# Kernel tuning notes

Measured on AMD Instinct MI355X. Metric: run time of the kernel, lower is better.

Reference implementation:

```python
import jax, jax.numpy as jnp
import numpy as np

NEG = -1e9  # effectively -inf for masked logits, grad-safe

def apply_rope(t, cos, sin):
    # t: [b, H, S, D]; cos/sin: [S, D] -> rotate-half RoPE
    d = t.shape[-1]
    t1, t2 = t[..., : d // 2], t[..., d // 2 :]
    rot = jnp.concatenate([-t2, t1], axis=-1)
    return t * cos[None, None] + rot * sin[None, None]


def setup_inputs() -> dict:
    key = jax.random.key(0)
    ks = jax.random.split(key, 8)
    b, S, d_in = 1, 4096, 2048
    H, G, D = 16, 4, 128
    d_out = H * D
    sc = 1.0 / np.sqrt(d_in)
    x = jax.random.normal(ks[0], (b, S, d_in), dtype=jnp.float32)
    # causal mask: True = masked (future positions)
    mask = jnp.triu(jnp.ones((S, S), dtype=bool), k=1)
    inv = 1.0 / (10000.0 ** (jnp.arange(0, D, 2, dtype=jnp.float32) / D))
    ang = jnp.arange(S, dtype=jnp.float32)[:, None] * inv[None, :]  # [S, D/2]
    ang = jnp.concatenate([ang, ang], axis=-1)                      # [S, D]
    cos, sin = jnp.cos(ang), jnp.sin(ang)
    Wq = jax.random.normal(ks[1], (d_out, d_in), dtype=jnp.float32) * sc
    Wk = jax.random.normal(ks[2], (G * D, d_in), dtype=jnp.float32) * sc
    Wv = jax.random.normal(ks[3], (G * D, d_in), dtype=jnp.float32) * sc
    Wo = jax.random.normal(ks[4], (d_in, d_out), dtype=jnp.float32) * sc
    return {"x": x, "mask": mask, "cos": cos, "sin": sin,
            "Wq": Wq, "Wk": Wk, "Wv": Wv, "Wo": Wo}


def reference(x, mask, cos, sin, Wq, Wk, Wv, Wo):
    b, S, d_in = x.shape
    G = Wk.shape[0] // cos.shape[-1]          # num_kv_groups
    D = cos.shape[-1]                          # head_dim
    H = Wq.shape[0] // D                       # num_heads
    n = H // G                                 # group_size
    q = (x @ Wq.T).reshape(b, S, H, D).transpose(0, 2, 1, 3)   # [b,H,S,D]
    k = (x @ Wk.T).reshape(b, S, G, D).transpose(0, 2, 1, 3)   # [b,G,S,D]
    v = (x @ Wv.T).reshape(b, S, G, D).transpose(0, 2, 1, 3)
    q = apply_rope(q, cos, sin)
    k = apply_rope(k, cos, sin)
    # GQA: group heads instead of repeat_interleave (head h -> group h // n)
    qg = q.reshape(b, G, n, S, D)
    scores = jnp.einsum('bgnqd,bgkd->bgnqk', qg, k)            # [b,G,n,S,S]
    scores = jnp.where(mask[None, None, None], NEG, scores)
    w = jax.nn.softmax(scores / np.sqrt(D), axis=-1)
    ctx = jnp.einsum('bgnqk,bgkd->bgnqd', w, v)                # [b,G,n,S,D]
    ctx = ctx.reshape(b, H, S, D).transpose(0, 2, 1, 3).reshape(b, S, H * D)
    return ctx @ Wo.T
```

## Files before the change

kernel.cpp:

```cpp
#include <hip/hip_runtime.h>

typedef __attribute__((ext_vector_type(8))) short bf16x8;
typedef __attribute__((ext_vector_type(4))) short bf16x4;
typedef __attribute__((ext_vector_type(8))) unsigned short u16x8;
typedef __attribute__((ext_vector_type(4))) float f32x4;

__device__ __forceinline__ unsigned short f2b(float f) {
  unsigned int u = __builtin_bit_cast(unsigned int, f);
  u += 0x7FFFu + ((u >> 16) & 1u);
  return (unsigned short)(u >> 16);
}
__device__ __forceinline__ float b2f(unsigned short h) {
  return __builtin_bit_cast(float, ((unsigned int)h) << 16);
}

__device__ __forceinline__ f32x4 mfma16x16x16(bf16x4 a, bf16x4 b, f32x4 c) {
#if __has_builtin(__builtin_amdgcn_mfma_f32_16x16x16bf16_1k)
  return __builtin_amdgcn_mfma_f32_16x16x16bf16_1k(a, b, c, 0, 0, 0);
#else
  asm volatile("v_mfma_f32_16x16x16_bf16 %0, %1, %2, %0" : "+v"(c) : "v"(a), "v"(b));
  return c;
#endif
}

#define AS1(p) (const __attribute__((address_space(1))) void*)(p)
#define AS3(p) (__attribute__((address_space(3))) void*)(p)

__device__ __forceinline__ void cvt8(const float* __restrict__ in,
                                     unsigned short* __restrict__ out,
                                     int i, float scale) {
  const float4* p = (const float4*)in + (size_t)i * 2;
  float4 a = p[0], b = p[1];
  u16x8 r;
  r[0] = f2b(a.x * scale); r[1] = f2b(a.y * scale);
  r[2] = f2b(a.z * scale); r[3] = f2b(a.w * scale);
  r[4] = f2b(b.x * scale); r[5] = f2b(b.y * scale);
  r[6] = f2b(b.z * scale); r[7] = f2b(b.w * scale);
  *((u16x8*)out + i) = r;
}

__global__ __launch_bounds__(256) void k_cvt_all(
    const float* __restrict__ x,  const float* __restrict__ Wq,
    const float* __restrict__ Wk, const float* __restrict__ Wv,
    const float* __restrict__ Wo, unsigned short* __restrict__ xb,
    unsigned short* __restrict__ wqkv, unsigned short* __restrict__ Wob,
    float sc) {
  int bid = blockIdx.x;
  int tid = threadIdx.x;
  if (bid < 4096)      cvt8(x,  xb,             (bid        ) * 256 + tid, 1.f);
  else if (bid < 6144) cvt8(Wq, wqkv,           (bid - 4096) * 256 + tid, sc);
  else if (bid < 6656) cvt8(Wk, wqkv + 4194304, (bid - 6144) * 256 + tid, 1.f);
  else if (bid < 7168) cvt8(Wv, wqkv + 5242880, (bid - 6656) * 256 + tid, 1.f);
  else                 cvt8(Wo, Wob,            (bid - 7168) * 256 + tid, 1.f);
}

__global__ __launch_bounds__(256) void k_post(unsigned short* __restrict__ qkv,
                                              const float* __restrict__ cosb,
                                              const float* __restrict__ sinb,
                                              unsigned short* __restrict__ vT) {
  __shared__ unsigned short tile[64][72];
  const int bid = blockIdx.x, t = threadIdx.x;
  if (bid < 2560) {
    int tid = bid * 256 + t;
    int oct = tid & 7;
    int hd  = (tid >> 3) % 20;
    int s   = (tid >> 3) / 20;
    unsigned short* p1 = qkv + (size_t)s * 3072 + hd * 128 + oct * 8;
    unsigned short* p2 = p1 + 64;
    u16x8 a = *(const u16x8*)p1;
    u16x8 b = *(const u16x8*)p2;
    const float4* cp = (const float4*)(cosb + (size_t)s * 128 + oct * 8);
    const float4* sp = (const float4*)(sinb + (size_t)s * 128 + oct * 8);
    float4 c0 = cp[0], c1 = cp[1], s0 = sp[0], s1 = sp[1];
    float cs[8] = {c0.x,c0.y,c0.z,c0.w,c1.x,c1.y,c1.z,c1.w};
    float sn[8] = {s0.x,s0.y,s0.z,s0.w,s1.x,s1.y,s1.z,s1.w};
    u16x8 ra, rb;
#pragma unroll
    for (int j = 0; j < 8; ++j) {
      float av = b2f(a[j]), bv = b2f(b[j]);
      ra[j] = f2b(av * cs[j] - bv * sn[j]);
      rb[j] = f2b(bv * cs[j] + av * sn[j]);
    }
    *(u16x8*)p1 = ra;
    *(u16x8*)p2 = rb;
  } else {
    int idx = bid - 2560;
    int bs = idx >> 3, bc = idx & 7;
#pragma unroll
    for (int i = 0; i < 2; ++i) {
      int c8 = t + 256 * i;
      int row = c8 >> 3, cb = c8 & 7;
      u16x8 v = *(const u16x8*)(qkv + (size_t)(bs * 64 + row) * 3072 + 2560 + bc * 64 + cb * 8);
#pragma unroll
      for (int j = 0; j < 8; ++j) tile[row][cb * 8 + j] = v[j];
    }
    __syncthreads();
#pragma unroll
    for (int i = 0; i < 2; ++i) {
      int c8 = t + 256 * i;
      int crow = c8 >> 3, sb = c8 & 7;
      u16x8 v;
#pragma unroll
      for (int j = 0; j < 8; ++j) v[j] = tile[sb * 8 + j][crow];
      *(u16x8*)(vT + (size_t)(bc * 64 + crow) * 4096 + bs * 64 + sb * 8) = v;
    }
  }
}

template <int OUTF32>
__global__ __launch_bounds__(256) void k_gemm_bt(
    const unsigned short* __restrict__ A, const unsigned short* __restrict__ B,
    void* __restrict__ C, int K, int lda, int ldb, int ldc) {
  __shared__ unsigned short As[128 * 64];
  __shared__ unsigned short Bs[128 * 64];
  const int t = threadIdx.x;
  const int lane = t & 63, w = t >> 6;
  const int wm = w >> 1, wn = w & 1;
  const int bn = blockIdx.x, bm = blockIdx.y;
  const unsigned short* Arow = A + (size_t)(bm * 128) * lda;
  const unsigned short* Brow = B + (size_t)(bn * 128) * ldb;

  f32x4 acc[4][4] = {};
  for (int kt = 0; kt < K; kt += 64) {
#pragma unroll
    for (int i = 0; i < 4; ++i) {
      int idx = i * 256 + t;
      int r = idx >> 3, blk = idx & 7;
      int sb = blk ^ (r & 7);
      __builtin_amdgcn_global_load_lds(AS1(Arow + (size_t)r * lda + kt + sb * 8),
                                       AS3(As + (i * 256 + w * 64) * 8), 16, 0, 0);
    }
#pragma unroll
    for (int i = 0; i < 4; ++i) {
      int idx = i * 256 + t;
      int r = idx >> 3, blk = idx & 7;
      int sb = blk ^ (r & 7);
      __builtin_amdgcn_global_load_lds(AS1(Brow + (size_t)r * ldb + kt + sb * 8),
                                       AS3(Bs + (i * 256 + w * 64) * 8), 16, 0, 0);
    }
    __syncthreads();
#pragma unroll
    for (int kk = 0; kk < 2; ++kk) {
      bf16x8 av[4], bv[4];
#pragma unroll
      for (int i = 0; i < 4; ++i) {
        int r = wm * 64 + i * 16 + (lane & 15);
        int off = (r * 128 + (kk * 32 + (lane >> 4) * 8) * 2) ^ ((r & 7) << 4);
        av[i] = *(const bf16x8*)((const char*)As + off);
      }
#pragma unroll
      for (int j = 0; j < 4; ++j) {
        int r = wn * 64 + j * 16 + (lane & 15);
        int off = (r * 128 + (kk * 32 + (lane >> 4) * 8) * 2) ^ ((r & 7) << 4);
        bv[j] = *(const bf16x8*)((const char*)Bs + off);
      }
#pragma unroll
      for (int i = 0; i < 4; ++i)
#pragma unroll
        for (int j = 0; j < 4; ++j)
          acc[i][j] = __builtin_amdgcn_mfma_f32_16x16x32_bf16(av[i], bv[j], acc[i][j], 0, 0, 0);
    }
    __syncthreads();
  }
#pragma unroll
  for (int i = 0; i < 4; ++i)
#pragma unroll
    for (int j = 0; j < 4; ++j)
#pragma unroll
      for (int r = 0; r < 4; ++r) {
        int m = bm * 128 + wm * 64 + i * 16 + (lane >> 4) * 4 + r;
        int n = bn * 128 + wn * 64 + j * 16 + (lane & 15);
        float v = acc[i][j][r];
        if (OUTF32) ((float*)C)[(size_t)m * ldc + n] = v;
        else        ((unsigned short*)C)[(size_t)m * ldc + n] = f2b(v);
      }
}

__device__ __forceinline__ void stage_k(const unsigned short* __restrict__ qk,
                                        unsigned short* __restrict__ dst,
                                        int kt, int g, int t, int w) {
#pragma unroll
  for (int i = 0; i < 4; ++i) {
    int idx = i * 256 + t;
    int r = idx >> 4, blk = idx & 15;
    int sb = (blk & 8) | ((blk ^ r) & 7);
    __builtin_amdgcn_global_load_lds(
        AS1(qk + (size_t)(kt * 64 + r) * 3072 + 2048 + g * 128 + sb * 8),
        AS3(dst + (i * 256 + w * 64) * 8), 16, 0, 0);
  }
}
__device__ __forceinline__ void stage_v(const unsigned short* __restrict__ vT,
                                        unsigned short* __restrict__ dst,
                                        int kt, int g, int t, int w) {
#pragma unroll
  for (int i = 0; i < 4; ++i) {
    int idx = i * 256 + t;
    int r = idx >> 3, blk = idx & 7;
    int sb = blk ^ (r & 7);
    __builtin_amdgcn_global_load_lds(
        AS1(vT + (size_t)(g * 128 + r) * 4096 + kt * 64 + sb * 8),
        AS3(dst + (i * 256 + w * 64) * 8), 16, 0, 0);
  }
}

__global__ __launch_bounds__(256, 1) void k_attn(const unsigned short* __restrict__ qk,
                                                 const unsigned short* __restrict__ vT,
                                                 unsigned short* __restrict__ ctx) {
  __shared__ unsigned short Ks[2][64 * 128];
  __shared__ unsigned short Vs[2][64 * 128];
  const int b = blockIdx.x;
  const int hp = blockIdx.y;
  const int h0 = hp * 2, g = hp >> 1;
  const int t = threadIdx.x, lane = t & 63, w = t >> 6;
  const int l15 = lane & 15, lq = lane >> 4;

  for (int ph = 0; ph < 2; ++ph) {
    const int qt = ph ? 63 - b : b;
    const int qg = qt * 64 + w * 16 + l15;

    bf16x8 aq0[4], aq1[4];
    {
      const unsigned short* qb =
          qk + (size_t)(qt * 64 + w * 16 + l15) * 3072 + h0 * 128 + lq * 8;
#pragma unroll
      for (int sl = 0; sl < 4; ++sl) {
        aq0[sl] = *(const bf16x8*)(qb + sl * 32);
        aq1[sl] = *(const bf16x8*)(qb + 128 + sl * 32);
      }
    }
    f32x4 o0[8] = {}, o1[8] = {};
    float lsum0 = 0.f, lsum1 = 0.f;

    stage_k(qk, Ks[0], 0, g, t, w);
    stage_v(vT, Vs[0], 0, g, t, w);
    asm volatile("s_waitcnt vmcnt(0)" ::: "memory");
    __builtin_amdgcn_s_barrier();

    auto tile = [&](const unsigned short* Kb, const unsigned short* Vb,
                    int kt, bool maskT) {
      f32x4 st0[4] = {}, st1[4] = {};
      __builtin_amdgcn_s_setprio(1);
#pragma unroll
      for (int sl = 0; sl < 4; ++sl)
#pragma unroll
        for (int nt = 0; nt < 4; ++nt) {
          int key = nt * 16 + l15;
          int off = (key * 256 + sl * 64 + lq * 16) ^ ((key & 7) << 4);
          bf16x8 bk = *(const bf16x8*)((const char*)Kb + off);
          st0[nt] = __builtin_amdgcn_mfma_f32_16x16x32_bf16(bk, aq0[sl], st0[nt], 0, 0, 0);
          st1[nt] = __builtin_amdgcn_mfma_f32_16x16x32_bf16(bk, aq1[sl], st1[nt], 0, 0, 0);
        }
      __builtin_amdgcn_s_setprio(0);

      bf16x4 pa0[4], pa1[4];
#pragma unroll
      for (int nt = 0; nt < 4; ++nt)
#pragma unroll
        for (int r = 0; r < 4; ++r) {
          float p0 = __builtin_amdgcn_exp2f(st0[nt][r]);
          float p1 = __builtin_amdgcn_exp2f(st1[nt][r]);
          if (maskT) {
            int key = kt * 64 + nt * 16 + lq * 4 + r;
            if (key > qg) { p0 = 0.f; p1 = 0.f; }
          }
          lsum0 += p0; lsum1 += p1;
          unsigned int u0 = __builtin_bit_cast(unsigned int, p0) + 0x8000u;
          unsigned int u1 = __builtin_bit_cast(unsigned int, p1) + 0x8000u;
          pa0[nt][r] = (short)(u0 >> 16);
          pa1[nt][r] = (short)(u1 >> 16);
        }

      __builtin_amdgcn_s_setprio(1);
#pragma unroll
      for (int nt = 0; nt < 4; ++nt)
#pragma unroll
        for (int dt = 0; dt < 8; ++dt) {
          int d = dt * 16 + l15;
          int off = (d * 128 + nt * 32 + lq * 8) ^ ((d & 7) << 4);
          bf16x4 vv = *(const bf16x4*)((const char*)Vb + off);
          o0[dt] = mfma16x16x16(pa0[nt], vv, o0[dt]);
          o1[dt] = mfma16x16x16(pa1[nt], vv, o1[dt]);
        }
      __builtin_amdgcn_s_setprio(0);
    };

    for (int kt = 0; kt < qt; ++kt) {
      const int cur = kt & 1;
      stage_k(qk, Ks[cur ^ 1], kt + 1, g, t, w);
      stage_v(vT, Vs[cur ^ 1], kt + 1, g, t, w);
      tile(Ks[cur], Vs[cur], kt, false);
      asm volatile("s_waitcnt vmcnt(0)" ::: "memory");
      __builtin_amdgcn_s_barrier();
    }
    {
      tile(Ks[qt & 1], Vs[qt & 1], qt, true);
      __builtin_amdgcn_s_barrier();
    }

    float f0 = lsum0, f1 = lsum1;
    f0 += __shfl_xor(f0, 16); f0 += __shfl_xor(f0, 32);
    f1 += __shfl_xor(f1, 16); f1 += __shfl_xor(f1, 32);
    float iq0[4], iq1[4];
#pragma unroll
    for (int r = 0; r < 4; ++r) {
      iq0[r] = 1.f / __shfl(f0, lq * 4 + r);
      iq1[r] = 1.f / __shfl(f1, lq * 4 + r);
    }
#pragma unroll
    for (int dt = 0; dt < 8; ++dt)
#pragma unroll
      for (int r = 0; r < 4; ++r) {
        int q = qt * 64 + w * 16 + lq * 4 + r;
        int c = h0 * 128 + dt * 16 + l15;
        ctx[(size_t)q * 2048 + c]       = f2b(o0[dt][r] * iq0[r]);
        ctx[(size_t)q * 2048 + c + 128] = f2b(o1[dt][r] * iq1[r]);
      }
  }
}

extern "C" void kernel_launch(void* const* d_in, const int* in_sizes, int n_in,
                              void* d_out, int out_size, void* d_ws, size_t ws_size,
                              hipStream_t stream) {
  const float* x    = (const float*)d_in[0];
  const float* cosb = (const float*)d_in[2];
  const float* sinb = (const float*)d_in[3];
  const float* Wq   = (const float*)d_in[4];
  const float* Wk   = (const float*)d_in[5];
  const float* Wv   = (const float*)d_in[6];
  const float* Wo   = (const float*)d_in[7];

  char* p = (char*)d_ws;
  unsigned short* xb   = (unsigned short*)p; p += (size_t)8388608 * 2;
  unsigned short* wqkv = (unsigned short*)p; p += (size_t)6291456 * 2;
  unsigned short* Wob  = (unsigned short*)p; p += (size_t)4194304 * 2;
  unsigned short* qkvb = (unsigned short*)p; p += (size_t)4096 * 3072 * 2;
  unsigned short* vTb  = (unsigned short*)p; p += (size_t)512 * 4096 * 2;
  unsigned short* ctx  = (unsigned short*)p; p += (size_t)4096 * 2048 * 2;
  if (ws_size < (size_t)(p - (char*)d_ws)) return;

  const float SC = 0.12751741f;

  k_cvt_all<<<9216, 256, 0, stream>>>(x, Wq, Wk, Wv, Wo, xb, wqkv, Wob, SC);

  k_gemm_bt<0><<<dim3(24, 32), 256, 0, stream>>>(xb, wqkv, qkvb, 2048, 2048, 2048, 3072);

  k_post<<<3072, 256, 0, stream>>>(qkvb, cosb, sinb, vTb);

  k_attn<<<dim3(32, 8), 256, 0, stream>>>(qkvb, vTb, ctx);

  k_gemm_bt<1><<<dim3(16, 32), 256, 0, stream>>>(ctx, Wob, d_out, 2048, 2048, 2048, 2048);
}
```

Measured before the change: 263.6 us.

## Process both paired causal query tiles concurrently with 512-thread attention blocks

The attention kernel now launches 512 threads per block, with waves 0-3 handling query tile b and waves 4-7 handling the paired tile 63-b at the same time, instead of processing the two tiles one after another. The K/V tiles staged into shared memory are loaded once and shared by both query tiles, which halves K/V global traffic for the short tile and doubles the waves available to hide latency. In exchange, the waves on the short tile sit idle at barriers once they pass their diagonal. Register pressure per wave is unchanged, but launch_bounds(512,1) may constrain the compiler's register allocation.

```diff
diff --git a/kernel.cpp b/kernel.cpp
--- a/kernel.cpp
+++ b/kernel.cpp
@@ -176,34 +176,34 @@
       }
 }
 
-__device__ __forceinline__ void stage_k(const unsigned short* __restrict__ qk,
-                                        unsigned short* __restrict__ dst,
-                                        int kt, int g, int t, int w) {
-#pragma unroll
-  for (int i = 0; i < 4; ++i) {
-    int idx = i * 256 + t;
+__device__ __forceinline__ void stage_k8(const unsigned short* __restrict__ qk,
+                                         unsigned short* __restrict__ dst,
+                                         int kt, int g, int t, int w) {
+#pragma unroll
+  for (int i = 0; i < 2; ++i) {
+    int idx = i * 512 + t;
     int r = idx >> 4, blk = idx & 15;
     int sb = (blk & 8) | ((blk ^ r) & 7);
     __builtin_amdgcn_global_load_lds(
         AS1(qk + (size_t)(kt * 64 + r) * 3072 + 2048 + g * 128 + sb * 8),
-        AS3(dst + (i * 256 + w * 64) * 8), 16, 0, 0);
-  }
-}
-__device__ __forceinline__ void stage_v(const unsigned short* __restrict__ vT,
-                                        unsigned short* __restrict__ dst,
-                                        int kt, int g, int t, int w) {
-#pragma unroll
-  for (int i = 0; i < 4; ++i) {
-    int idx = i * 256 + t;
+        AS3(dst + (i * 512 + w * 64) * 8), 16, 0, 0);
+  }
+}
+__device__ __forceinline__ void stage_v8(const unsigned short* __restrict__ vT,
+                                         unsigned short* __restrict__ dst,
+                                         int kt, int g, int t, int w) {
+#pragma unroll
+  for (int i = 0; i < 2; ++i) {
+    int idx = i * 512 + t;
     int r = idx >> 3, blk = idx & 7;
     int sb = blk ^ (r & 7);
     __builtin_amdgcn_global_load_lds(
         AS1(vT + (size_t)(g * 128 + r) * 4096 + kt * 64 + sb * 8),
-        AS3(dst + (i * 256 + w * 64) * 8), 16, 0, 0);
-  }
-}
-
-__global__ __launch_bounds__(256, 1) void k_attn(const unsigned short* __restrict__ qk,
+        AS3(dst + (i * 512 + w * 64) * 8), 16, 0, 0);
+  }
+}
+
+__global__ __launch_bounds__(512, 1) void k_attn(const unsigned short* __restrict__ qk,
                                                  const unsigned short* __restrict__ vT,
                                                  unsigned short* __restrict__ ctx) {
   __shared__ unsigned short Ks[2][64 * 128];
@@ -212,110 +212,108 @@
   const int hp = blockIdx.y;
   const int h0 = hp * 2, g = hp >> 1;
   const int t = threadIdx.x, lane = t & 63, w = t >> 6;
+  const int wq = w & 3;
+  const int myqt = (w < 4) ? b : 63 - b;
+  const int kmax = 63 - b;
   const int l15 = lane & 15, lq = lane >> 4;
-
-  for (int ph = 0; ph < 2; ++ph) {
-    const int qt = ph ? 63 - b : b;
-    const int qg = qt * 64 + w * 16 + l15;
-
-    bf16x8 aq0[4], aq1[4];
-    {
-      const unsigned short* qb =
-          qk + (size_t)(qt * 64 + w * 16 + l15) * 3072 + h0 * 128 + lq * 8;
-#pragma unroll
-      for (int sl = 0; sl < 4; ++sl) {
-        aq0[sl] = *(const bf16x8*)(qb + sl * 32);
-        aq1[sl] = *(const bf16x8*)(qb + 128 + sl * 32);
-      }
-    }
-    f32x4 o0[8] = {}, o1[8] = {};
-    float lsum0 = 0.f, lsum1 = 0.f;
-
-    stage_k(qk, Ks[0], 0, g, t, w);
-    stage_v(vT, Vs[0], 0, g, t, w);
+  const int qg = myqt * 64 + wq * 16 + l15;
+
+  bf16x8 aq0[4], aq1[4];
+  {
+    const unsigned short* qb =
+        qk + (size_t)(myqt * 64 + wq * 16 + l15) * 3072 + h0 * 128 + lq * 8;
+#pragma unroll
+    for (int sl = 0; sl < 4; ++sl) {
+      aq0[sl] = *(const bf16x8*)(qb + sl * 32);
+      aq1[sl] = *(const bf16x8*)(qb + 128 + sl * 32);
+    }
+  }
+  f32x4 o0[8] = {}, o1[8] = {};
+  float lsum0 = 0.f, lsum1 = 0.f;
+
+  stage_k8(qk, Ks[0], 0, g, t, w);
+  stage_v8(vT, Vs[0], 0, g, t, w);
+  asm volatile("s_waitcnt vmcnt(0)" ::: "memory");
+  __builtin_amdgcn_s_barrier();
+
+  auto tile = [&](const unsigned short* Kb, const unsigned short* Vb,
+                  int kt, bool maskT) {
+    f32x4 st0[4] = {}, st1[4] = {};
+    __builtin_amdgcn_s_setprio(1);
+#pragma unroll
+    for (int sl = 0; sl < 4; ++sl)
+#pragma unroll
+      for (int nt = 0; nt < 4; ++nt) {
+        int key = nt * 16 + l15;
+        int off = (key * 256 + sl * 64 + lq * 16) ^ ((key & 7) << 4);
+        bf16x8 bk = *(const bf16x8*)((const char*)Kb + off);
+        st0[nt] = __builtin_amdgcn_mfma_f32_16x16x32_bf16(bk, aq0[sl], st0[nt], 0, 0, 0);
+        st1[nt] = __builtin_amdgcn_mfma_f32_16x16x32_bf16(bk, aq1[sl], st1[nt], 0, 0, 0);
+      }
+    __builtin_amdgcn_s_setprio(0);
+
+    bf16x4 pa0[4], pa1[4];
+#pragma unroll
+    for (int nt = 0; nt < 4; ++nt)
+#pragma unroll
+      for (int r = 0; r < 4; ++r) {
+        float p0 = __builtin_amdgcn_exp2f(st0[nt][r]);
+        float p1 = __builtin_amdgcn_exp2f(st1[nt][r]);
+        if (maskT) {
+          int key = kt * 64 + nt * 16 + lq * 4 + r;
+          if (key > qg) { p0 = 0.f; p1 = 0.f; }
+        }
+        lsum0 += p0; lsum1 += p1;
+        unsigned int u0 = __builtin_bit_cast(unsigned int, p0) + 0x8000u;
+        unsigned int u1 = __builtin_bit_cast(unsigned int, p1) + 0x8000u;
+        pa0[nt][r] = (short)(u0 >> 16);
+        pa1[nt][r] = (short)(u1 >> 16);
+      }
+
+    __builtin_amdgcn_s_setprio(1);
+#pragma unroll
+    for (int nt = 0; nt < 4; ++nt)
+#pragma unroll
+      for (int dt = 0; dt < 8; ++dt) {
+        int d = dt * 16 + l15;
+        int off = (d * 128 + nt * 32 + lq * 8) ^ ((d & 7) << 4);
+        bf16x4 vv = *(const bf16x4*)((const char*)Vb + off);
+        o0[dt] = mfma16x16x16(pa0[nt], vv, o0[dt]);
+        o1[dt] = mfma16x16x16(pa1[nt], vv, o1[dt]);
+      }
+    __builtin_amdgcn_s_setprio(0);
+  };
+
+  for (int kt = 0; kt <= kmax; ++kt) {
+    const int cur = kt & 1;
+    if (kt < kmax) {
+      stage_k8(qk, Ks[cur ^ 1], kt + 1, g, t, w);
+      stage_v8(vT, Vs[cur ^ 1], kt + 1, g, t, w);
+    }
+    if (kt <= myqt)
+      tile(Ks[cur], Vs[cur], kt, kt == myqt);
     asm volatile("s_waitcnt vmcnt(0)" ::: "memory");
     __builtin_amdgcn_s_barrier();
-
-    auto tile = [&](const unsigned short* Kb, const unsigned short* Vb,
-                    int kt, bool maskT) {
-      f32x4 st0[4] = {}, st1[4] = {};
-      __builtin_amdgcn_s_setprio(1);
-#pragma unroll
-      for (int sl = 0; sl < 4; ++sl)
-#pragma unroll
-        for (int nt = 0; nt < 4; ++nt) {
-          int key = nt * 16 + l15;
-          int off = (key * 256 + sl * 64 + lq * 16) ^ ((key & 7) << 4);
-          bf16x8 bk = *(const bf16x8*)((const char*)Kb + off);
-          st0[nt] = __builtin_amdgcn_mfma_f32_16x16x32_bf16(bk, aq0[sl], st0[nt], 0, 0, 0);
-          st1[nt] = __builtin_amdgcn_mfma_f32_16x16x32_bf16(bk, aq1[sl], st1[nt], 0, 0, 0);
-        }
-      __builtin_amdgcn_s_setprio(0);
-
-      bf16x4 pa0[4], pa1[4];
-#pragma unroll
-      for (int nt = 0; nt < 4; ++nt)
-#pragma unroll
-        for (int r = 0; r < 4; ++r) {
-          float p0 = __builtin_amdgcn_exp2f(st0[nt][r]);
-          float p1 = __builtin_amdgcn_exp2f(st1[nt][r]);
-          if (maskT) {
-            int key = kt * 64 + nt * 16 + lq * 4 + r;
-            if (key > qg) { p0 = 0.f; p1 = 0.f; }
-          }
-          lsum0 += p0; lsum1 += p1;
-          unsigned int u0 = __builtin_bit_cast(unsigned int, p0) + 0x8000u;
-          unsigned int u1 = __builtin_bit_cast(unsigned int, p1) + 0x8000u;
-          pa0[nt][r] = (short)(u0 >> 16);
-          pa1[nt][r] = (short)(u1 >> 16);
-        }
-
-      __builtin_amdgcn_s_setprio(1);
-#pragma unroll
-      for (int nt = 0; nt < 4; ++nt)
-#pragma unroll
-        for (int dt = 0; dt < 8; ++dt) {
-          int d = dt * 16 + l15;
-          int off = (d * 128 + nt * 32 + lq * 8) ^ ((d & 7) << 4);
-          bf16x4 vv = *(const bf16x4*)((const char*)Vb + off);
-          o0[dt] = mfma16x16x16(pa0[nt], vv, o0[dt]);
-          o1[dt] = mfma16x16x16(pa1[nt], vv, o1[dt]);
-        }
-      __builtin_amdgcn_s_setprio(0);
-    };
-
-    for (int kt = 0; kt < qt; ++kt) {
-      const int cur = kt & 1;
-      stage_k(qk, Ks[cur ^ 1], kt + 1, g, t, w);
-      stage_v(vT, Vs[cur ^ 1], kt + 1, g, t, w);
-      tile(Ks[cur], Vs[cur], kt, false);
-      asm volatile("s_waitcnt vmcnt(0)" ::: "memory");
-      __builtin_amdgcn_s_barrier();
-    }
-    {
-      tile(Ks[qt & 1], Vs[qt & 1], qt, true);
-      __builtin_amdgcn_s_barrier();
-    }
-
-    float f0 = lsum0, f1 = lsum1;
-    f0 += __shfl_xor(f0, 16); f0 += __shfl_xor(f0, 32);
-    f1 += __shfl_xor(f1, 16); f1 += __shfl_xor(f1, 32);
-    float iq0[4], iq1[4];
+  }
+
+  float f0 = lsum0, f1 = lsum1;
+  f0 += __shfl_xor(f0, 16); f0 += __shfl_xor(f0, 32);
+  f1 += __shfl_xor(f1, 16); f1 += __shfl_xor(f1, 32);
+  float iq0[4], iq1[4];
+#pragma unroll
+  for (int r = 0; r < 4; ++r) {
+    iq0[r] = 1.f / __shfl(f0, lq * 4 + r);
+    iq1[r] = 1.f / __shfl(f1, lq * 4 + r);
+  }
+#pragma unroll
+  for (int dt = 0; dt < 8; ++dt)
 #pragma unroll
     for (int r = 0; r < 4; ++r) {
-      iq0[r] = 1.f / __shfl(f0, lq * 4 + r);
-      iq1[r] = 1.f / __shfl(f1, lq * 4 + r);
-    }
-#pragma unroll
-    for (int dt = 0; dt < 8; ++dt)
-#pragma unroll
-      for (int r = 0; r < 4; ++r) {
-        int q = qt * 64 + w * 16 + lq * 4 + r;
-        int c = h0 * 128 + dt * 16 + l15;
-        ctx[(size_t)q * 2048 + c]       = f2b(o0[dt][r] * iq0[r]);
-        ctx[(size_t)q * 2048 + c + 128] = f2b(o1[dt][r] * iq1[r]);
-      }
-  }
+      int q = myqt * 64 + wq * 16 + lq * 4 + r;
+      int c = h0 * 128 + dt * 16 + l15;
+      ctx[(size_t)q * 2048 + c]       = f2b(o0[dt][r] * iq0[r]);
+      ctx[(size_t)q * 2048 + c + 128] = f2b(o1[dt][r] * iq1[r]);
+    }
 }
 
 extern "C" void kernel_launch(void* const* d_in, const int* in_sizes, int n_in,
@@ -346,7 +344,7 @@
 
   k_post<<<3072, 256, 0, stream>>>(qkvb, cosb, sinb, vTb);
 
-  k_attn<<<dim3(32, 8), 256, 0, stream>>>(qkvb, vTb, ctx);
+  k_attn<<<dim3(32, 8), 512, 0, stream>>>(qkvb, vTb, ctx);
 
   k_gemm_bt<1><<<dim3(16, 32), 256, 0, stream>>>(ctx, Wob, d_out, 2048, 2048, 2048, 2048);
 }
```

New measurement: 271.4 us. 1.03x slower.

## Split attention key range across two warp groups per block with LDS reduction

Applied to the files above, without the earlier changes.

Doubles the attention block to 512 threads. Two groups of four waves each process half of the key tiles for the same query tile, with separate double-buffered K/V shared memory. Partial outputs and row sums from the second group go through LDS to the first group, which normalizes and writes ctx. This is meant to raise per-CU parallelism, since only 256 blocks run on a many-CU device. The cost is twice the LDS, an extra reduction pass and more barriers. It relies on the softmax having no running max, so the partial sums can simply be added.

```diff
diff --git a/kernel.cpp b/kernel.cpp
--- a/kernel.cpp
+++ b/kernel.cpp
@@ -203,25 +203,36 @@
   }
 }
 
-__global__ __launch_bounds__(256, 1) void k_attn(const unsigned short* __restrict__ qk,
+__global__ __launch_bounds__(512, 1) void k_attn(const unsigned short* __restrict__ qk,
                                                  const unsigned short* __restrict__ vT,
                                                  unsigned short* __restrict__ ctx) {
-  __shared__ unsigned short Ks[2][64 * 128];
-  __shared__ unsigned short Vs[2][64 * 128];
+  __shared__ unsigned short Ks[2][2][64 * 128];
+  __shared__ unsigned short Vs[2][2][64 * 128];
   const int b = blockIdx.x;
   const int hp = blockIdx.y;
   const int h0 = hp * 2, g = hp >> 1;
-  const int t = threadIdx.x, lane = t & 63, w = t >> 6;
+  const int t = threadIdx.x;
+  const int grp = t >> 8;
+  const int tg = t & 255;
+  const int lane = t & 63, w4 = (t >> 6) & 3;
   const int l15 = lane & 15, lq = lane >> 4;
+
+  float* ol = (float*)&Ks[0][0][0];
+  float* ll = (float*)&Vs[0][0][0];
 
   for (int ph = 0; ph < 2; ++ph) {
     const int qt = ph ? 63 - b : b;
-    const int qg = qt * 64 + w * 16 + l15;
+    const int ntot = qt + 1;
+    const int m = (ntot + 1) >> 1;
+    const int nB = ntot - m;
+    const int kbase = grp ? m : 0;
+    const int ntile = grp ? nB : m;
+    const int qg = qt * 64 + w4 * 16 + l15;
 
     bf16x8 aq0[4], aq1[4];
     {
       const unsigned short* qb =
-          qk + (size_t)(qt * 64 + w * 16 + l15) * 3072 + h0 * 128 + lq * 8;
+          qk + (size_t)(qt * 64 + w4 * 16 + l15) * 3072 + h0 * 128 + lq * 8;
 #pragma unroll
       for (int sl = 0; sl < 4; ++sl) {
         aq0[sl] = *(const bf16x8*)(qb + sl * 32);
@@ -231,8 +242,15 @@
     f32x4 o0[8] = {}, o1[8] = {};
     float lsum0 = 0.f, lsum1 = 0.f;
 
-    stage_k(qk, Ks[0], 0, g, t, w);
-    stage_v(vT, Vs[0], 0, g, t, w);
+    unsigned short* K0 = Ks[grp][0];
+    unsigned short* K1 = Ks[grp][1];
+    unsigned short* V0 = Vs[grp][0];
+    unsigned short* V1 = Vs[grp][1];
+
+    if (ntile > 0) {
+      stage_k(qk, K0, kbase, g, tg, w4);
+      stage_v(vT, V0, kbase, g, tg, w4);
+    }
     asm volatile("s_waitcnt vmcnt(0)" ::: "memory");
     __builtin_amdgcn_s_barrier();
 
@@ -284,37 +302,65 @@
       __builtin_amdgcn_s_setprio(0);
     };
 
-    for (int kt = 0; kt < qt; ++kt) {
-      const int cur = kt & 1;
-      stage_k(qk, Ks[cur ^ 1], kt + 1, g, t, w);
-      stage_v(vT, Vs[cur ^ 1], kt + 1, g, t, w);
-      tile(Ks[cur], Vs[cur], kt, false);
+    for (int i = 0; i < m; ++i) {
+      const int cur = i & 1;
+      if (i + 1 < ntile) {
+        stage_k(qk, cur ? K0 : K1, kbase + i + 1, g, tg, w4);
+        stage_v(vT, cur ? V0 : V1, kbase + i + 1, g, tg, w4);
+      }
+      if (i < ntile) {
+        const int kt = kbase + i;
+        tile(cur ? K1 : K0, cur ? V1 : V0, kt, kt == qt);
+      }
       asm volatile("s_waitcnt vmcnt(0)" ::: "memory");
-      __builtin_amdgcn_s_barrier();
-    }
-    {
-      tile(Ks[qt & 1], Vs[qt & 1], qt, true);
       __builtin_amdgcn_s_barrier();
     }
 
     float f0 = lsum0, f1 = lsum1;
     f0 += __shfl_xor(f0, 16); f0 += __shfl_xor(f0, 32);
     f1 += __shfl_xor(f1, 16); f1 += __shfl_xor(f1, 32);
-    float iq0[4], iq1[4];
-#pragma unroll
-    for (int r = 0; r < 4; ++r) {
-      iq0[r] = 1.f / __shfl(f0, lq * 4 + r);
-      iq1[r] = 1.f / __shfl(f1, lq * 4 + r);
-    }
-#pragma unroll
-    for (int dt = 0; dt < 8; ++dt)
+
+    if (grp == 1) {
+#pragma unroll
+      for (int dt = 0; dt < 8; ++dt)
+#pragma unroll
+        for (int r = 0; r < 4; ++r) {
+          ol[(dt * 4 + r) * 256 + tg]        = o0[dt][r];
+          ol[(32 + dt * 4 + r) * 256 + tg]   = o1[dt][r];
+        }
+      if (lq == 0) {
+        ll[w4 * 16 + l15]      = f0;
+        ll[64 + w4 * 16 + l15] = f1;
+      }
+    }
+    __builtin_amdgcn_s_barrier();
+    if (grp == 0) {
+#pragma unroll
+      for (int dt = 0; dt < 8; ++dt)
+#pragma unroll
+        for (int r = 0; r < 4; ++r) {
+          o0[dt][r] += ol[(dt * 4 + r) * 256 + tg];
+          o1[dt][r] += ol[(32 + dt * 4 + r) * 256 + tg];
+        }
+      f0 += ll[w4 * 16 + l15];
+      f1 += ll[64 + w4 * 16 + l15];
+      float iq0[4], iq1[4];
 #pragma unroll
       for (int r = 0; r < 4; ++r) {
-        int q = qt * 64 + w * 16 + lq * 4 + r;
-        int c = h0 * 128 + dt * 16 + l15;
-        ctx[(size_t)q * 2048 + c]       = f2b(o0[dt][r] * iq0[r]);
-        ctx[(size_t)q * 2048 + c + 128] = f2b(o1[dt][r] * iq1[r]);
-      }
+        iq0[r] = 1.f / __shfl(f0, lq * 4 + r);
+        iq1[r] = 1.f / __shfl(f1, lq * 4 + r);
+      }
+#pragma unroll
+      for (int dt = 0; dt < 8; ++dt)
+#pragma unroll
+        for (int r = 0; r < 4; ++r) {
+          int q = qt * 64 + w4 * 16 + lq * 4 + r;
+          int c = h0 * 128 + dt * 16 + l15;
+          ctx[(size_t)q * 2048 + c]       = f2b(o0[dt][r] * iq0[r]);
+          ctx[(size_t)q * 2048 + c + 128] = f2b(o1[dt][r] * iq1[r]);
+        }
+    }
+    __builtin_amdgcn_s_barrier();
   }
 }
 
@@ -346,7 +392,7 @@
 
   k_post<<<3072, 256, 0, stream>>>(qkvb, cosb, sinb, vTb);
 
-  k_attn<<<dim3(32, 8), 256, 0, stream>>>(qkvb, vTb, ctx);
+  k_attn<<<dim3(32, 8), 512, 0, stream>>>(qkvb, vTb, ctx);
 
   k_gemm_bt<1><<<dim3(16, 32), 256, 0, stream>>>(ctx, Wob, d_out, 2048, 2048, 2048, 2048);
 }
```

After: 234.5 us. 11.0% less time.
